# Performance work log

Measured on AMD Instinct MI355X. Metric: run time of the kernel, lower is better.

The kernel has to match this reference:

```python
import jax, jax.numpy as jnp
import numpy as np

WH = WW = 7          # window size
N_TOK = WH * WW      # 49 tokens per window
HEADS = 8
HEAD_DIM = 32
DIM = HEADS * HEAD_DIM  # 256
NW = 64              # windows per image (56x56 / 7x7)
BW = 64 * NW         # batch_images * windows = 4096


def _rel_pos_index(wh, ww):
    # Swin-style relative position index, flattened to (N*N,)
    coords = np.stack(np.meshgrid(np.arange(wh), np.arange(ww), indexing='ij'))  # (2, wh, ww)
    coords = coords.reshape(2, -1)                                               # (2, N)
    rel = coords[:, :, None] - coords[:, None, :]                                # (2, N, N)
    rel = rel.transpose(1, 2, 0).astype(np.int64)                                # (N, N, 2)
    rel[:, :, 0] += wh - 1
    rel[:, :, 1] += ww - 1
    rel[:, :, 0] *= 2 * ww - 1
    return jnp.asarray(rel.sum(-1).reshape(-1))                                  # (N*N,)

_REL_IDX = _rel_pos_index(WH, WW)


def setup_inputs() -> dict:
    key = jax.random.key(0)
    ks = jax.random.split(key, 5)
    x = jax.random.normal(ks[0], (BW, N_TOK, DIM), dtype=jnp.float32)
    mask = jnp.zeros((1, NW, 1, N_TOK, N_TOK), dtype=jnp.float32)
    w_qkv = jax.random.normal(ks[1], (DIM, 3 * HEADS * HEAD_DIM), dtype=jnp.float32) * 0.02
    b_qkv = jnp.zeros((3 * HEADS * HEAD_DIM,), dtype=jnp.float32)
    rel_table = jax.random.normal(ks[2], ((2 * WH - 1) * (2 * WW - 1), HEADS), dtype=jnp.float32) * 0.02
    w_out = jax.random.normal(ks[3], (HEADS * HEAD_DIM, DIM), dtype=jnp.float32) * 0.02
    b_out = jnp.zeros((DIM,), dtype=jnp.float32)
    return {"x": x, "mask": mask, "w_qkv": w_qkv, "b_qkv": b_qkv,
            "rel_table": rel_table, "w_out": w_out, "b_out": b_out}


def reference(x, mask, w_qkv, b_qkv, rel_table, w_out, b_out):
    bw, n, d = x.shape
    # QKV projection then split per original Rearrange:
    # 'b n (qkv h hd) -> qkv b h n hd'
    qkv = (x @ w_qkv + b_qkv).reshape(bw, n, 3, HEADS, HEAD_DIM)
    qkv = qkv.transpose(2, 0, 3, 1, 4)  # (3, bw, h, n, hd)
    q, k, v = qkv[0], qkv[1], qkv[2]
    # NOTE: original computes einsum('bnid,bnjd->bnij', k, q): a[i,j] = k_i . q_j
    a = jnp.einsum('bhid,bhjd->bhij', k, q) / jnp.sqrt(jnp.asarray(HEAD_DIM, x.dtype))
    # relative position bias: table gather then '(i j) h -> h i j'
    bias = rel_table[_REL_IDX].reshape(n, n, HEADS).transpose(2, 0, 1)  # (h, n, n)
    a = a + bias
    # mask add: '(b nW) h i j -> b nW h i j', + mask, back
    nw = mask.shape[1]
    a = a.reshape(bw // nw, nw, HEADS, n, n) + mask
    a = a.reshape(bw, HEADS, n, n)
    a = jax.nn.softmax(a, axis=-1)
    y = jnp.einsum('bhij,bhjd->bhid', a, v)        # (bw, h, n, hd)
    y = y.transpose(0, 2, 1, 3).reshape(bw, n, HEADS * HEAD_DIM)
    return y @ w_out + b_out
```

## Files before the change

### kernel.cpp

```cpp
#include <hip/hip_runtime.h>

typedef __attribute__((ext_vector_type(8))) short short8;
typedef __attribute__((ext_vector_type(4))) float f32x4;
typedef unsigned short u16;

#define NTOK 49
#define NBLK 4096
#define LOG2E 1.4426950408889634f

#define XF  0
#define QKP 16384
#define VTF 49152
#define POOLN 65536

#define WS_WQT 0
#define WS_WOT 393216
#define WS_BQS 524288
#define WS_BIAS 528384
#define WS_MKG 659456
#define WS_CMB 1708032
#define WS_NEED (WS_CMB + 8388608)

__device__ __forceinline__ u16 f2bf(float f) {
  unsigned u = __float_as_uint(f);
  return (u16)((u + 0x7fffu + ((u >> 16) & 1u)) >> 16);
}
__device__ __forceinline__ unsigned packbf(float a, float b) {
  unsigned r;
  asm("v_cvt_pk_bf16_f32 %0, %1, %2" : "=v"(r) : "v"(a), "v"(b));
  return r;
}

__device__ __forceinline__ short8 asm_frag(unsigned c0p0, unsigned c0p1,
                                           unsigned c1p0, unsigned c1p1,
                                           int srcA, int srcB, bool cSel) {
  unsigned a0 = (unsigned)__shfl((int)c0p0, srcA);
  unsigned b0 = (unsigned)__shfl((int)c1p0, srcA);
  unsigned a1 = (unsigned)__shfl((int)c0p1, srcA);
  unsigned b1 = (unsigned)__shfl((int)c1p1, srcA);
  unsigned a2 = (unsigned)__shfl((int)c0p0, srcB);
  unsigned b2 = (unsigned)__shfl((int)c1p0, srcB);
  unsigned a3 = (unsigned)__shfl((int)c0p1, srcB);
  unsigned b3 = (unsigned)__shfl((int)c1p1, srcB);
  union { unsigned u[4]; short8 s8; } r;
  r.u[0] = cSel ? b0 : a0;
  r.u[1] = cSel ? b1 : a1;
  r.u[2] = cSel ? b2 : a2;
  r.u[3] = cSel ? b3 : a3;
  return r.s8;
}

__global__ void prep_kernel(const float* __restrict__ w_qkv,
                            const float* __restrict__ w_out,
                            const float* __restrict__ rel,
                            const float* __restrict__ mask,
                            const float* __restrict__ b_qkv,
                            u16* __restrict__ wqTf,
                            u16* __restrict__ woTf,
                            float* __restrict__ bqs,
                            float* __restrict__ biasf,
                            float* __restrict__ mkg) {
  const float SCQ = 0.17677669529663687f * LOG2E;
  const int stride = gridDim.x * blockDim.x;
  const int gid = blockIdx.x * blockDim.x + threadIdx.x;
  for (int e = gid; e < 48 * 8 * 64 * 8; e += stride) {
    int eL = e & 7, ln = (e >> 3) & 63, ks = (e >> 9) & 7, ctg = e >> 12;
    int k = ks * 32 + (ln >> 4) * 8 + eL;
    int c = ctg * 16 + (ln & 15);
    float wv = w_qkv[k * 768 + c];
    if (ctg < 16) wv *= SCQ;
    wqTf[e] = f2bf(wv);
  }
  for (int e = gid; e < 16 * 8 * 64 * 8; e += stride) {
    int eL = e & 7, ln = (e >> 3) & 63, ks = (e >> 9) & 7, ctg = e >> 12;
    int k = ks * 32 + (ln >> 4) * 8 + eL;
    int c = ctg * 16 + (ln & 15);
    woTf[e] = f2bf(w_out[k * 256 + c]);
  }
  for (int e = gid; e < 768; e += stride)
    bqs[e] = b_qkv[e] * (e < 256 ? SCQ : 1.f);
  for (int e = gid; e < 8 * 16 * 64 * 4; e += stride) {
    int rg = e & 3, ln = (e >> 2) & 63, t = (e >> 8) & 15, hh = e >> 12;
    int i = (t >> 2) * 16 + (ln & 15);
    int j = (t & 3) * 16 + (ln >> 4) * 4 + rg;
    float v;
    if (j >= NTOK) v = -1e30f;
    else if (i >= NTOK) v = 0.f;
    else {
      int dh = i / 7 - j / 7 + 6;
      int dw = i % 7 - j % 7 + 6;
      v = rel[(dh * 13 + dw) * 8 + hh];
    }
    biasf[e] = v * LOG2E;
  }
  for (int e = gid; e < 64 * 16 * 64 * 4; e += stride) {
    int rg = e & 3, ln = (e >> 2) & 63, t = (e >> 8) & 15, wdw = e >> 12;
    int i = (t >> 2) * 16 + (ln & 15);
    int j = (t & 3) * 16 + (ln >> 4) * 4 + rg;
    mkg[e] = (i < NTOK && j < NTOK) ? mask[wdw * (NTOK * NTOK) + i * NTOK + j] * LOG2E : 0.f;
  }
}

__global__ void prep2_kernel(const float* __restrict__ biasf,
                             const float* __restrict__ mkg,
                             float* __restrict__ cmb) {
  const int stride = gridDim.x * blockDim.x;
  for (int e = blockIdx.x * blockDim.x + threadIdx.x; e < 64 * 8 * 4096; e += stride) {
    int x = e & 4095, hh = (e >> 12) & 7, wdw = e >> 15;
    cmb[e] = biasf[hh * 4096 + x] + mkg[wdw * 4096 + x];
  }
}

__global__ void __launch_bounds__(1024, 4) winattn_mfma(
    const float* __restrict__ x,
    const float* __restrict__ bqs,
    const float* __restrict__ b_out,
    const u16* __restrict__ wqTf,
    const u16* __restrict__ woTf,
    const float* __restrict__ biasf,
    const float* __restrict__ mkg,
    const float* __restrict__ cmb,
    float* __restrict__ out)
{
  __shared__ u16 pool[POOLN];
  const int b = blockIdx.x, tid = threadIdx.x;
  const int lane = tid & 63, lo = lane & 15, hi = lane >> 4;
  const int w = tid >> 6;
  const int h = w & 7;
  const int it0 = (w >> 3) * 2;
  const f32x4 zf = {0.f, 0.f, 0.f, 0.f};

  {
    const float4* xg = (const float4*)(x + (size_t)b * (NTOK * 256));
    for (int e = tid; e < 49 * 64; e += 1024) {
      float4 v = xg[e];
      int r = e >> 6, c4 = (e & 63) << 2;
      int addr = (((r >> 4) * 8 + (c4 >> 5)) * 64 + ((c4 >> 3) & 3) * 16 + (r & 15)) * 8 + (c4 & 7);
      *(uint2*)&pool[XF + addr] = make_uint2(packbf(v.x, v.y), packbf(v.z, v.w));
    }
    if (tid < 15 * 64) {
      int e = tid;
      int r = 49 + (e >> 6), c4 = (e & 63) << 2;
      int addr = (((r >> 4) * 8 + (c4 >> 5)) * 64 + ((c4 >> 3) & 3) * 16 + (r & 15)) * 8 + (c4 & 7);
      *(uint2*)&pool[XF + addr] = make_uint2(0u, 0u);
    }
  }
  __syncthreads();

  {
    const int ctq0 = 2 * w, ctq1 = 2 * w + 1, ctv = 32 + w;
    f32x4 acc[3][4];
    #pragma unroll
    for (int ct = 0; ct < 3; ++ct)
      #pragma unroll
      for (int rt = 0; rt < 4; ++rt) acc[ct][rt] = zf;
    #pragma unroll
    for (int ks = 0; ks < 8; ++ks) {
      short8 bx[4];
      #pragma unroll
      for (int rt = 0; rt < 4; ++rt)
        bx[rt] = *(const short8*)&pool[XF + ((rt * 8 + ks) * 64 + lane) * 8];
      short8 af0 = *(const short8*)&wqTf[((size_t)(ctq0 * 8 + ks) * 64 + lane) * 8];
      short8 af1 = *(const short8*)&wqTf[((size_t)(ctq1 * 8 + ks) * 64 + lane) * 8];
      short8 afv = *(const short8*)&wqTf[((size_t)(ctv * 8 + ks) * 64 + lane) * 8];
      #pragma unroll
      for (int rt = 0; rt < 4; ++rt) {
        acc[0][rt] = __builtin_amdgcn_mfma_f32_16x16x32_bf16(af0, bx[rt], acc[0][rt], 0, 0, 0);
        acc[1][rt] = __builtin_amdgcn_mfma_f32_16x16x32_bf16(af1, bx[rt], acc[1][rt], 0, 0, 0);
        acc[2][rt] = __builtin_amdgcn_mfma_f32_16x16x32_bf16(bx[rt], afv, acc[2][rt], 0, 0, 0);
      }
    }
    const int qkbase = QKP + (w & 7) * 4096 + ((w >= 8) ? 2048 : 0);
    #pragma unroll
    for (int ct = 0; ct < 2; ++ct) {
      const int ctg = 2 * w + ct;
      f32x4 bias = *(const f32x4*)(bqs + ctg * 16 + hi * 4);
      #pragma unroll
      for (int rt = 0; rt < 4; ++rt) {
        f32x4 v = acc[ct][rt] + bias;
        int hi2 = ct * 2 + (hi >> 1);
        int eb = (hi & 1) * 4;
        *(uint2*)&pool[qkbase + (rt * 64 + hi2 * 16 + lo) * 8 + eb] =
            make_uint2(packbf(v[0], v[1]), packbf(v[2], v[3]));
      }
    }
    {
      const int vhead = w >> 1, dblk = w & 1;
      const float bv = bqs[ctv * 16 + lo];
      #pragma unroll
      for (int rt = 0; rt < 4; ++rt) {
        f32x4 v = acc[2][rt];
        float v0 = v[0] + bv, v1 = v[1] + bv, v2 = v[2] + bv, v3 = v[3] + bv;
        int f = dblk * 2 + (rt >> 1);
        int hiR = (rt & 1) * 2 + (hi >> 1);
        int eb = (hi & 1) * 4;
        *(uint2*)&pool[VTF + (f * 8 + vhead) * 512 + (hiR * 16 + lo) * 8 + eb] =
            make_uint2(packbf(v0, v1), packbf(v2, v3));
      }
    }
  }
  __syncthreads();

  float rs0 = 0.f, rs1 = 0.f;
  unsigned pkp[4][2][2];
  {
    short8 ka0 = *(const short8*)&pool[QKP + h * 4096 + 2048 + ((it0 + 0) * 64 + lane) * 8];
    short8 ka1 = *(const short8*)&pool[QKP + h * 4096 + 2048 + ((it0 + 1) * 64 + lane) * 8];
    const float* cb;
    const float* mb = nullptr;
    if (cmb) {
      cb = cmb + (((size_t)(b & 63) * 8 + h) << 12);
    } else {
      cb = biasf + h * 4096;
      mb = mkg + (size_t)(b & 63) * 4096;
    }
    #pragma unroll
    for (int jt = 0; jt < 4; ++jt) {
      short8 qa = *(const short8*)&pool[QKP + h * 4096 + (jt * 64 + lane) * 8];
      f32x4 s0 = __builtin_amdgcn_mfma_f32_16x16x32_bf16(qa, ka0, zf, 0, 0, 0);
      f32x4 s1 = __builtin_amdgcn_mfma_f32_16x16x32_bf16(qa, ka1, zf, 0, 0, 0);
      {
        const int t = (it0 + 0) * 4 + jt;
        f32x4 c4 = *(const f32x4*)&cb[(t * 64 + lane) * 4];
        if (mb) {
          f32x4 m4 = *(const f32x4*)&mb[(t * 64 + lane) * 4];
          c4[0] += m4[0]; c4[1] += m4[1]; c4[2] += m4[2]; c4[3] += m4[3];
        }
        float p0 = exp2f(s0[0] + c4[0]);
        float p1 = exp2f(s0[1] + c4[1]);
        float p2 = exp2f(s0[2] + c4[2]);
        float p3 = exp2f(s0[3] + c4[3]);
        rs0 += (p0 + p1) + (p2 + p3);
        pkp[jt][0][0] = packbf(p0, p1);
        pkp[jt][0][1] = packbf(p2, p3);
      }
      {
        const int t = (it0 + 1) * 4 + jt;
        f32x4 c4 = *(const f32x4*)&cb[(t * 64 + lane) * 4];
        if (mb) {
          f32x4 m4 = *(const f32x4*)&mb[(t * 64 + lane) * 4];
          c4[0] += m4[0]; c4[1] += m4[1]; c4[2] += m4[2]; c4[3] += m4[3];
        }
        float p0 = exp2f(s1[0] + c4[0]);
        float p1 = exp2f(s1[1] + c4[1]);
        float p2 = exp2f(s1[2] + c4[2]);
        float p3 = exp2f(s1[3] + c4[3]);
        rs1 += (p0 + p1) + (p2 + p3);
        pkp[jt][1][0] = packbf(p0, p1);
        pkp[jt][1][1] = packbf(p2, p3);
      }
    }
  }
  float inv0, inv1;
  {
    float r2 = rs0 + __shfl_xor(rs0, 16);
    inv0 = 1.f / (r2 + __shfl_xor(r2, 32));
    float r3 = rs1 + __shfl_xor(rs1, 16);
    inv1 = 1.f / (r3 + __shfl_xor(r3, 32));
  }

  {
    const int srcA = lo + 32 * (hi & 1);
    const int srcB = srcA + 16;
    const bool cSel = (hi & 2) != 0;
    short8 va[2][2];
    #pragma unroll
    for (int dblk = 0; dblk < 2; ++dblk)
      #pragma unroll
      for (int k2 = 0; k2 < 2; ++k2)
        va[dblk][k2] = *(const short8*)&pool[VTF + ((dblk * 2 + k2) * 8 + h) * 512 + lane * 8];
    f32x4 ya[2][2];
    ya[0][0] = zf; ya[0][1] = zf; ya[1][0] = zf; ya[1][1] = zf;
    #pragma unroll
    for (int itL = 0; itL < 2; ++itL)
      #pragma unroll
      for (int k2 = 0; k2 < 2; ++k2) {
        short8 pb = asm_frag(pkp[2 * k2][itL][0], pkp[2 * k2][itL][1],
                             pkp[2 * k2 + 1][itL][0], pkp[2 * k2 + 1][itL][1], srcA, srcB, cSel);
        ya[0][itL] = __builtin_amdgcn_mfma_f32_16x16x32_bf16(va[0][k2], pb, ya[0][itL], 0, 0, 0);
        ya[1][itL] = __builtin_amdgcn_mfma_f32_16x16x32_bf16(va[1][k2], pb, ya[1][itL], 0, 0, 0);
      }
    #pragma unroll
    for (int itL = 0; itL < 2; ++itL) {
      const float iv = itL ? inv1 : inv0;
      #pragma unroll
      for (int dblk = 0; dblk < 2; ++dblk) {
        f32x4 yy = ya[dblk][itL];
        int hi2 = dblk * 2 + (hi >> 1);
        int eb = (hi & 1) * 4;
        *(uint2*)&pool[XF + (((it0 + itL) * 8 + h) * 64 + hi2 * 16 + lo) * 8 + eb] =
            make_uint2(packbf(yy[0] * iv, yy[1] * iv), packbf(yy[2] * iv, yy[3] * iv));
      }
    }
  }
  __syncthreads();

  {
    f32x4 pacc[4];
    pacc[0] = zf; pacc[1] = zf; pacc[2] = zf; pacc[3] = zf;
    #pragma unroll
    for (int ks = 0; ks < 8; ++ks) {
      short8 wf = *(const short8*)&woTf[((size_t)(w * 8 + ks) * 64 + lane) * 8];
      #pragma unroll
      for (int rt = 0; rt < 4; ++rt) {
        short8 yb = *(const short8*)&pool[XF + ((rt * 8 + ks) * 64 + lane) * 8];
        pacc[rt] = __builtin_amdgcn_mfma_f32_16x16x32_bf16(wf, yb, pacc[rt], 0, 0, 0);
      }
    }
    float* og = out + (size_t)b * (NTOK * 256);
    const int cb2 = w * 16 + hi * 4;
    f32x4 bb = *(const f32x4*)(b_out + cb2);
    #pragma unroll
    for (int rt = 0; rt < 4; ++rt) {
      const int r = rt * 16 + lo;
      if (r < NTOK) {
        f32x4 vv = pacc[rt] + bb;
        *(f32x4*)(og + (size_t)r * 256 + cb2) = vv;
      }
    }
  }
}

extern "C" void kernel_launch(void* const* d_in, const int* in_sizes, int n_in,
                              void* d_out, int out_size, void* d_ws, size_t ws_size,
                              hipStream_t stream) {
  const float *x = nullptr, *mask = nullptr, *w_qkv = nullptr, *b_qkv = nullptr,
              *rel_t = nullptr, *w_out = nullptr, *b_out = nullptr;
  for (int i = 0; i < n_in; ++i) {
    const float* p = (const float*)d_in[i];
    switch (in_sizes[i]) {
      case 4096 * 49 * 256: x = p; break;
      case 64 * 49 * 49:    mask = p; break;
      case 256 * 768:       w_qkv = p; break;
      case 768:             b_qkv = p; break;
      case 169 * 8:         rel_t = p; break;
      case 256 * 256:       w_out = p; break;
      case 256:             b_out = p; break;
    }
  }
  char* wsb = (char*)d_ws;
  u16* wqTf    = (u16*)(wsb + WS_WQT);
  u16* woTf    = (u16*)(wsb + WS_WOT);
  float* bqs   = (float*)(wsb + WS_BQS);
  float* biasf = (float*)(wsb + WS_BIAS);
  float* mkg   = (float*)(wsb + WS_MKG);
  const bool fits = (ws_size >= (size_t)WS_NEED);
  float* cmb   = fits ? (float*)(wsb + WS_CMB) : nullptr;

  hipLaunchKernelGGL(prep_kernel, dim3(1024), dim3(256), 0, stream,
                     w_qkv, w_out, rel_t, mask, b_qkv, wqTf, woTf, bqs, biasf, mkg);
  if (fits) {
    hipLaunchKernelGGL(prep2_kernel, dim3(2048), dim3(256), 0, stream,
                       biasf, mkg, cmb);
  }
  hipLaunchKernelGGL(winattn_mfma, dim3(NBLK), dim3(1024), 0, stream,
                     x, bqs, b_out, wqTf, woTf, biasf, mkg, cmb, (float*)d_out);
}
```

Before: 282.2 us.

## Switch QKV projection to 32x32x16 MFMA with per-head wave tiling

```diff
diff --git a/kernel.cpp b/kernel.cpp
--- a/kernel.cpp
+++ b/kernel.cpp
@@ -2,6 +2,7 @@
 
 typedef __attribute__((ext_vector_type(8))) short short8;
 typedef __attribute__((ext_vector_type(4))) float f32x4;
+typedef __attribute__((ext_vector_type(16))) float f32x16;
 typedef unsigned short u16;
 
 #define NTOK 49
@@ -63,12 +64,12 @@
   const float SCQ = 0.17677669529663687f * LOG2E;
   const int stride = gridDim.x * blockDim.x;
   const int gid = blockIdx.x * blockDim.x + threadIdx.x;
-  for (int e = gid; e < 48 * 8 * 64 * 8; e += stride) {
-    int eL = e & 7, ln = (e >> 3) & 63, ks = (e >> 9) & 7, ctg = e >> 12;
-    int k = ks * 32 + (ln >> 4) * 8 + eL;
-    int c = ctg * 16 + (ln & 15);
+  for (int e = gid; e < 24 * 16 * 64 * 8; e += stride) {
+    int eL = e & 7, ln = (e >> 3) & 63, ks = (e >> 9) & 15, ctg = e >> 13;
+    int k = ks * 16 + (ln >> 5) * 8 + eL;
+    int c = ctg * 32 + (ln & 31);
     float wv = w_qkv[k * 768 + c];
-    if (ctg < 16) wv *= SCQ;
+    if (c < 256) wv *= SCQ;
     wqTf[e] = f2bf(wv);
   }
   for (int e = gid; e < 16 * 8 * 64 * 8; e += stride) {
@@ -135,66 +136,62 @@
     for (int e = tid; e < 49 * 64; e += 1024) {
       float4 v = xg[e];
       int r = e >> 6, c4 = (e & 63) << 2;
-      int addr = (((r >> 4) * 8 + (c4 >> 5)) * 64 + ((c4 >> 3) & 3) * 16 + (r & 15)) * 8 + (c4 & 7);
+      int tt = r >> 5, ln = (r & 31) + 32 * ((c4 >> 3) & 1), ks = c4 >> 4;
+      int addr = ((tt * 16 + ks) * 64 + ln) * 8 + (c4 & 7);
       *(uint2*)&pool[XF + addr] = make_uint2(packbf(v.x, v.y), packbf(v.z, v.w));
     }
     if (tid < 15 * 64) {
       int e = tid;
       int r = 49 + (e >> 6), c4 = (e & 63) << 2;
-      int addr = (((r >> 4) * 8 + (c4 >> 5)) * 64 + ((c4 >> 3) & 3) * 16 + (r & 15)) * 8 + (c4 & 7);
+      int tt = r >> 5, ln = (r & 31) + 32 * ((c4 >> 3) & 1), ks = c4 >> 4;
+      int addr = ((tt * 16 + ks) * 64 + ln) * 8 + (c4 & 7);
       *(uint2*)&pool[XF + addr] = make_uint2(0u, 0u);
     }
   }
   __syncthreads();
 
   {
-    const int ctq0 = 2 * w, ctq1 = 2 * w + 1, ctv = 32 + w;
-    f32x4 acc[3][4];
-    #pragma unroll
-    for (int ct = 0; ct < 3; ++ct)
-      #pragma unroll
-      for (int rt = 0; rt < 4; ++rt) acc[ct][rt] = zf;
-    #pragma unroll
-    for (int ks = 0; ks < 8; ++ks) {
-      short8 bx[4];
-      #pragma unroll
-      for (int rt = 0; rt < 4; ++rt)
-        bx[rt] = *(const short8*)&pool[XF + ((rt * 8 + ks) * 64 + lane) * 8];
-      short8 af0 = *(const short8*)&wqTf[((size_t)(ctq0 * 8 + ks) * 64 + lane) * 8];
-      short8 af1 = *(const short8*)&wqTf[((size_t)(ctq1 * 8 + ks) * 64 + lane) * 8];
-      short8 afv = *(const short8*)&wqTf[((size_t)(ctv * 8 + ks) * 64 + lane) * 8];
-      #pragma unroll
-      for (int rt = 0; rt < 4; ++rt) {
-        acc[0][rt] = __builtin_amdgcn_mfma_f32_16x16x32_bf16(af0, bx[rt], acc[0][rt], 0, 0, 0);
-        acc[1][rt] = __builtin_amdgcn_mfma_f32_16x16x32_bf16(af1, bx[rt], acc[1][rt], 0, 0, 0);
-        acc[2][rt] = __builtin_amdgcn_mfma_f32_16x16x32_bf16(bx[rt], afv, acc[2][rt], 0, 0, 0);
-      }
-    }
-    const int qkbase = QKP + (w & 7) * 4096 + ((w >= 8) ? 2048 : 0);
-    #pragma unroll
-    for (int ct = 0; ct < 2; ++ct) {
-      const int ctg = 2 * w + ct;
-      f32x4 bias = *(const f32x4*)(bqs + ctg * 16 + hi * 4);
-      #pragma unroll
-      for (int rt = 0; rt < 4; ++rt) {
-        f32x4 v = acc[ct][rt] + bias;
-        int hi2 = ct * 2 + (hi >> 1);
-        int eb = (hi & 1) * 4;
-        *(uint2*)&pool[qkbase + (rt * 64 + hi2 * 16 + lo) * 8 + eb] =
-            make_uint2(packbf(v[0], v[1]), packbf(v[2], v[3]));
-      }
+    const int hq = w & 7, tt = w >> 3;
+    const int ls = hi >> 1;
+    f32x16 accq = {0.f,0.f,0.f,0.f,0.f,0.f,0.f,0.f,0.f,0.f,0.f,0.f,0.f,0.f,0.f,0.f};
+    f32x16 acck = accq, accv = accq;
+    #pragma unroll
+    for (int ks = 0; ks < 16; ++ks) {
+      short8 bx = *(const short8*)&pool[XF + ((tt * 16 + ks) * 64 + lane) * 8];
+      short8 wq = *(const short8*)&wqTf[((size_t)((0  + hq) * 16 + ks) * 64 + lane) * 8];
+      short8 wk = *(const short8*)&wqTf[((size_t)((8  + hq) * 16 + ks) * 64 + lane) * 8];
+      short8 wv = *(const short8*)&wqTf[((size_t)((16 + hq) * 16 + ks) * 64 + lane) * 8];
+      accq = __builtin_amdgcn_mfma_f32_32x32x16_bf16(wq, bx, accq, 0, 0, 0);
+      acck = __builtin_amdgcn_mfma_f32_32x32x16_bf16(wk, bx, acck, 0, 0, 0);
+      accv = __builtin_amdgcn_mfma_f32_32x32x16_bf16(bx, wv, accv, 0, 0, 0);
     }
     {
-      const int vhead = w >> 1, dblk = w & 1;
-      const float bv = bqs[ctv * 16 + lo];
-      #pragma unroll
-      for (int rt = 0; rt < 4; ++rt) {
-        f32x4 v = acc[2][rt];
-        float v0 = v[0] + bv, v1 = v[1] + bv, v2 = v[2] + bv, v3 = v[3] + bv;
-        int f = dblk * 2 + (rt >> 1);
-        int hiR = (rt & 1) * 2 + (hi >> 1);
-        int eb = (hi & 1) * 4;
-        *(uint2*)&pool[VTF + (f * 8 + vhead) * 512 + (hiR * 16 + lo) * 8 + eb] =
+      const int t = tt * 32 + (lane & 31);
+      const int ubase = ((t >> 4) * 64 + (t & 15)) * 8 + 4 * ls;
+      #pragma unroll
+      for (int q2 = 0; q2 < 4; ++q2) {
+        f32x4 bq4 = *(const f32x4*)(bqs + hq * 32 + q2 * 8 + ls * 4);
+        f32x4 bk4 = *(const f32x4*)(bqs + 256 + hq * 32 + q2 * 8 + ls * 4);
+        float q0 = accq[4*q2+0] + bq4[0], q1 = accq[4*q2+1] + bq4[1];
+        float q2v = accq[4*q2+2] + bq4[2], q3 = accq[4*q2+3] + bq4[3];
+        float k0 = acck[4*q2+0] + bk4[0], k1 = acck[4*q2+1] + bk4[1];
+        float k2v = acck[4*q2+2] + bk4[2], k3 = acck[4*q2+3] + bk4[3];
+        *(uint2*)&pool[QKP + hq * 4096 + ubase + 16 * q2 * 8] =
+            make_uint2(packbf(q0, q1), packbf(q2v, q3));
+        *(uint2*)&pool[QKP + hq * 4096 + 2048 + ubase + 16 * q2 * 8] =
+            make_uint2(packbf(k0, k1), packbf(k2v, k3));
+      }
+    }
+    {
+      const int dv = lane & 31;
+      const float bv = bqs[512 + hq * 32 + dv];
+      const int slot = ((dv >> 4) * 2 + tt) * 8 + hq;
+      const int vbase = slot * 512 + (dv & 15) * 8 + 4 * ls;
+      #pragma unroll
+      for (int q2 = 0; q2 < 4; ++q2) {
+        float v0 = accv[4*q2+0] + bv, v1 = accv[4*q2+1] + bv;
+        float v2 = accv[4*q2+2] + bv, v3 = accv[4*q2+3] + bv;
+        *(uint2*)&pool[VTF + vbase + 16 * q2 * 8] =
             make_uint2(packbf(v0, v1), packbf(v2, v3));
       }
     }
```

Measured after the change: 318.6 us. +12.9%, slower.
